# Kernel optimization log

Hardware: AMD Instinct MI355X
Metric: run time of the kernel (lower is better)

The kernel has to match this reference:

```python
import jax, jax.numpy as jnp
import numpy as np

B, C, HIMG, WIMG = 32, 3, 224, 224
P, D, L, F, H, NC = 16, 768, 12, 3072, 12, 1000
S = (HIMG // P) * (WIMG // P)  # 196 tokens
DH = D // H                    # 64 per head


def setup_inputs() -> dict:
    key = jax.random.key(0)
    ks = jax.random.split(key, 12)
    rn = lambda i, shape, sc: jax.random.normal(ks[i], shape, jnp.float32) * sc
    return dict(
        x=rn(0, (B, C, HIMG, WIMG), 1.0),
        conv_w=rn(1, (D, C, P, P), 0.02),
        conv_b=jnp.zeros((D,), jnp.float32),
        pos_embed=rn(2, (S, D), 0.02),
        ln1_s=jnp.ones((L, D), jnp.float32),
        ln1_b=jnp.zeros((L, D), jnp.float32),
        wq=rn(3, (L, D, D), 0.02),
        wk=rn(4, (L, D, D), 0.02),
        wv=rn(5, (L, D, D), 0.02),
        ln2_s=jnp.ones((L, D), jnp.float32),
        ln2_b=jnp.zeros((L, D), jnp.float32),
        w1=rn(6, (L, D, F), 0.02),
        b1=jnp.zeros((L, F), jnp.float32),
        w2=rn(7, (L, F, D), 0.02),
        b2=jnp.zeros((L, D), jnp.float32),
        fc_w=rn(8, (D, NC), 0.02),
        fc_b=jnp.zeros((NC,), jnp.float32),
    )


def _layernorm(x, scale, bias, eps=1e-5):
    m = x.mean(-1, keepdims=True)
    v = ((x - m) ** 2).mean(-1, keepdims=True)
    return (x - m) * jax.lax.rsqrt(v + eps) * scale + bias


def reference(x, conv_w, conv_b, pos_embed, ln1_s, ln1_b, wq, wk, wv,
              ln2_s, ln2_b, w1, b1, w2, b2, fc_w, fc_b):
    # patch embedding: stride-P conv, then b c h w -> b (h w) c, add pos embed
    h = jax.lax.conv_general_dilated(
        x, conv_w, (P, P), 'VALID',
        dimension_numbers=('NCHW', 'OIHW', 'NCHW'))
    h = h + conv_b[None, :, None, None]
    h = h.reshape(B, D, S).transpose(0, 2, 1) + pos_embed  # [B,S,D]

    # NOTE: original scales attention logits by 1/sqrt(seq_len), not 1/sqrt(d_head)
    scale = 1.0 / jnp.sqrt(jnp.float32(S))

    def layer(hx, p):
        l1s, l1b, Wq, Wk, Wv, l2s, l2b, W1, B1, W2, B2 = p
        xn = _layernorm(hx, l1s, l1b)
        q = (xn @ Wq).reshape(B, S, H, DH)
        k = (xn @ Wk).reshape(B, S, H, DH)
        v = (xn @ Wv).reshape(B, S, H, DH)
        att = jax.nn.softmax(jnp.einsum('bshd,bthd->bhst', q, k) * scale, axis=-1)
        o = jnp.einsum('bhst,bthd->bshd', att, v).reshape(B, S, D)
        hx = hx + o
        y = _layernorm(hx, l2s, l2b) @ W1 + B1
        y = jax.nn.gelu(y, approximate=False) @ W2 + B2
        return hx + y, None

    h, _ = jax.lax.scan(layer, h, (ln1_s, ln1_b, wq, wk, wv,
                                   ln2_s, ln2_b, w1, b1, w2, b2))
    return h.mean(axis=1) @ fc_w + fc_b  # [B, num_classes]
```

## Files before the change

kernel.cpp:

```cpp
#include <hip/hip_runtime.h>
#include <hip/hip_bf16.h>

typedef __attribute__((ext_vector_type(8))) short bf16x8;
typedef __attribute__((ext_vector_type(4))) short bf16x4;
typedef __attribute__((ext_vector_type(4))) float f32x4;

#define DEVI static __device__ __forceinline__

DEVI unsigned short f2bf(float f) {
  __hip_bfloat16 h = __float2bfloat16(f);
  return __builtin_bit_cast(unsigned short, h);
}

DEVI f32x4 mfma16(bf16x8 a, bf16x8 b, f32x4 c) {
  return __builtin_amdgcn_mfma_f32_16x16x32_bf16(a, b, c, 0, 0, 0);
}

DEVI void gload16(const unsigned short* g, unsigned short* l) {
  __builtin_amdgcn_global_load_lds(
      (const __attribute__((address_space(1))) void*)g,
      (__attribute__((address_space(3))) void*)l, 16, 0, 0);
}

__global__ __launch_bounds__(256) void k_im2col(const float* __restrict__ x,
                                                unsigned short* __restrict__ A) {
  int t = blockIdx.x * 256 + threadIdx.x;
  int m = t / 192;
  int qq = t - m * 192;
  int kk = qq * 4;
  int c = kk >> 8;
  int r = kk & 255;
  int i = r >> 4;
  int j = r & 15;
  int b = m / 196;
  int s = m - b * 196;
  int ph = s / 14;
  int pw = s - ph * 14;
  const float* src = x + ((size_t)((b * 3 + c) * 224 + ph * 16 + i)) * 224 + pw * 16 + j;
  f32x4 v = *reinterpret_cast<const f32x4*>(src);
  bf16x4 o;
  o[0] = (short)f2bf(v[0]); o[1] = (short)f2bf(v[1]);
  o[2] = (short)f2bf(v[2]); o[3] = (short)f2bf(v[3]);
  *reinterpret_cast<bf16x4*>(A + (size_t)m * 768 + kk) = o;
}

__global__ __launch_bounds__(256) void k_cvt(const float* __restrict__ in,
                                             unsigned short* __restrict__ out) {
  int t = blockIdx.x * 256 + threadIdx.x;
  f32x4 v = *reinterpret_cast<const f32x4*>(in + (size_t)t * 4);
  bf16x4 o;
  o[0] = (short)f2bf(v[0]); o[1] = (short)f2bf(v[1]);
  o[2] = (short)f2bf(v[2]); o[3] = (short)f2bf(v[3]);
  *reinterpret_cast<bf16x4*>(out + (size_t)t * 4) = o;
}

DEVI void transpose_tile(const float* __restrict__ in, unsigned short* __restrict__ out,
                         int K, int N, int kt, int nt, unsigned short (*tile)[68]) {
  int r = threadIdx.x >> 4;
  int c4 = (threadIdx.x & 15) * 4;
  int k0 = kt * 64, n0 = nt * 64;
#pragma unroll
  for (int rr0 = 0; rr0 < 4; rr0++) {
    int rr = r + rr0 * 16;
    f32x4 v = *reinterpret_cast<const f32x4*>(in + (size_t)(k0 + rr) * N + n0 + c4);
    bf16x4 o;
    o[0] = (short)f2bf(v[0]); o[1] = (short)f2bf(v[1]);
    o[2] = (short)f2bf(v[2]); o[3] = (short)f2bf(v[3]);
    *reinterpret_cast<bf16x4*>(&tile[rr][c4]) = o;
  }
  __syncthreads();
#pragma unroll
  for (int rr0 = 0; rr0 < 4; rr0++) {
    int rr = r + rr0 * 16;
    bf16x4 o;
    o[0] = (short)tile[c4 + 0][rr];
    o[1] = (short)tile[c4 + 1][rr];
    o[2] = (short)tile[c4 + 2][rr];
    o[3] = (short)tile[c4 + 3][rr];
    *reinterpret_cast<bf16x4*>(out + (size_t)(n0 + rr) * K + k0 + c4) = o;
  }
}

__global__ __launch_bounds__(256) void k_wconvert(
    const float* __restrict__ wq, const float* __restrict__ wk, const float* __restrict__ wv,
    const float* __restrict__ w1, const float* __restrict__ w2,
    unsigned short* __restrict__ wqkvT, unsigned short* __restrict__ w1T,
    unsigned short* __restrict__ w2T) {
  __shared__ unsigned short tile[64][68];
  int bid = blockIdx.x;
  if (bid < 432) {
    int mm = bid / 144, t2 = bid - mm * 144;
    const float* in = (mm == 0) ? wq : ((mm == 1) ? wk : wv);
    transpose_tile(in, wqkvT + (size_t)mm * 768 * 768, 768, 768, t2 / 12, t2 % 12, tile);
  } else if (bid < 1008) {
    int t2 = bid - 432;
    transpose_tile(w1, w1T, 768, 3072, t2 / 48, t2 % 48, tile);
  } else {
    int t2 = bid - 1008;
    transpose_tile(w2, w2T, 3072, 768, t2 / 12, t2 % 12, tile);
  }
}

__global__ __launch_bounds__(256) void k_ln(const float* __restrict__ h,
                                            const float* __restrict__ sc,
                                            const float* __restrict__ bi,
                                            unsigned short* __restrict__ xn) {
  int wave = threadIdx.x >> 6, lane = threadIdx.x & 63;
  int row = blockIdx.x * 4 + wave;
  const float* hr = h + (size_t)row * 768;
  f32x4 v[3];
  float sum = 0.f;
#pragma unroll
  for (int i = 0; i < 3; i++) {
    v[i] = *reinterpret_cast<const f32x4*>(hr + i * 256 + lane * 4);
    sum += v[i][0] + v[i][1] + v[i][2] + v[i][3];
  }
#pragma unroll
  for (int m = 1; m < 64; m <<= 1) sum += __shfl_xor(sum, m, 64);
  float mean = sum * (1.f / 768.f);
  float var = 0.f;
#pragma unroll
  for (int i = 0; i < 3; i++)
#pragma unroll
    for (int c = 0; c < 4; c++) { float d = v[i][c] - mean; var += d * d; }
#pragma unroll
  for (int m = 1; m < 64; m <<= 1) var += __shfl_xor(var, m, 64);
  float rs = rsqrtf(var * (1.f / 768.f) + 1e-5f);
#pragma unroll
  for (int i = 0; i < 3; i++) {
    int col = i * 256 + lane * 4;
    f32x4 s4 = *reinterpret_cast<const f32x4*>(sc + col);
    f32x4 b4 = *reinterpret_cast<const f32x4*>(bi + col);
    bf16x4 o;
#pragma unroll
    for (int c = 0; c < 4; c++) o[c] = (short)f2bf((v[i][c] - mean) * rs * s4[c] + b4[c]);
    *reinterpret_cast<bf16x4*>(xn + (size_t)row * 768 + col) = o;
  }
}

template <int EPI>
__global__ __launch_bounds__(256) void k_gemm(
    const unsigned short* __restrict__ A, const unsigned short* __restrict__ Bt, int K,
    const float* __restrict__ bias, const float* __restrict__ aux,
    float* __restrict__ outF, unsigned short* __restrict__ outB) {
  __shared__ __align__(16) unsigned short As[128 * 32];
  __shared__ __align__(16) unsigned short Bs[128 * 32];
  int m0 = blockIdx.y * 128, n0 = blockIdx.x * 128;
  int tid = threadIdx.x;
  int wave = tid >> 6, lane = tid & 63;
  int wm = (wave >> 1) * 64, wn = (wave & 1) * 64;
  int lr = lane & 15, lg = lane >> 4;

  f32x4 acc[4][4];
  const f32x4 fz = {0.f, 0.f, 0.f, 0.f};
#pragma unroll
  for (int i = 0; i < 4; i++)
#pragma unroll
    for (int j = 0; j < 4; j++) acc[i][j] = fz;

  int srow = wave * 16 + (lane >> 2);
  int scol = (lane & 3) * 8;
  const unsigned short* Ag = A + (size_t)(m0 + srow) * K + scol;
  const unsigned short* Bg = Bt + (size_t)(n0 + srow) * K + scol;
  unsigned short* Al = &As[wave * 16 * 32];
  unsigned short* Bl = &Bs[wave * 16 * 32];

  int nk = K >> 5;
  for (int kt = 0; kt < nk; kt++) {
    int k0 = kt << 5;
#pragma unroll
    for (int j = 0; j < 2; j++) {
      gload16(Ag + (size_t)j * 64 * K + k0, Al + j * 64 * 32);
      gload16(Bg + (size_t)j * 64 * K + k0, Bl + j * 64 * 32);
    }
    __syncthreads();
    bf16x8 a[4], b[4];
#pragma unroll
    for (int i = 0; i < 4; i++) {
      a[i] = *reinterpret_cast<const bf16x8*>(&As[(wm + i * 16 + lr) * 32 + lg * 8]);
      b[i] = *reinterpret_cast<const bf16x8*>(&Bs[(wn + i * 16 + lr) * 32 + lg * 8]);
    }
#pragma unroll
    for (int mi = 0; mi < 4; mi++)
#pragma unroll
      for (int ni = 0; ni < 4; ni++) acc[mi][ni] = mfma16(a[mi], b[ni], acc[mi][ni]);
    __syncthreads();
  }

#pragma unroll
  for (int mi = 0; mi < 4; mi++) {
#pragma unroll
    for (int ni = 0; ni < 4; ni++) {
#pragma unroll
      for (int r = 0; r < 4; r++) {
        int m = m0 + wm + mi * 16 + lg * 4 + r;
        int n = n0 + wn + ni * 16 + lr;
        float val = acc[mi][ni][r];
        if (EPI == 0) {
          int s = m % 196;
          outF[(size_t)m * 768 + n] = val + bias[n] + aux[(size_t)s * 768 + n];
        } else if (EPI == 1) {
          int bb = m / 196, s = m - bb * 196;
          int which = n / 768, n7 = n - which * 768;
          int hd = n7 >> 6, dh = n7 & 63;
          outB[(size_t)which * 4816896 + ((size_t)((bb * 12 + hd) * 196 + s) << 6) + dh] =
              f2bf(val);
        } else if (EPI == 2) {
          float tt = val + bias[n];
          float g = 0.5f * tt * (1.f + erff(tt * 0.70710678118654752f));
          outB[(size_t)m * 3072 + n] = f2bf(g);
        } else {
          outF[(size_t)m * 768 + n] += val + bias[n];
        }
      }
    }
  }
}

__global__ __launch_bounds__(256) void k_attn(const unsigned short* __restrict__ q,
                                              const unsigned short* __restrict__ k,
                                              const unsigned short* __restrict__ v,
                                              float* __restrict__ h) {
  __shared__ __align__(16) unsigned short Kl[208][72];
  __shared__ __align__(16) unsigned short Vt[64][248];
  __shared__ __align__(16) unsigned short Sc[4][16][232];
  int bh = blockIdx.x;
  int b = bh / 12, hh = bh - b * 12;
  size_t base = (size_t)bh * 196 * 64;
  int tid = threadIdx.x, wave = tid >> 6, lane = tid & 63;
  int lr = lane & 15, lg = lane >> 4;

  const bf16x8 bz = {0, 0, 0, 0, 0, 0, 0, 0};
  for (int u = tid; u < 208 * 8; u += 256) {
    int row = u >> 3, c8 = (u & 7) * 8;
    bf16x8 val = bz;
    if (row < 196) val = *reinterpret_cast<const bf16x8*>(k + base + row * 64 + c8);
    *reinterpret_cast<bf16x8*>(&Kl[row][c8]) = val;
  }
  for (int u = tid; u < 224 * 8; u += 256) {
    int t = u >> 3, d8 = (u & 7) * 8;
    bf16x8 val = bz;
    if (t < 196) val = *reinterpret_cast<const bf16x8*>(v + base + t * 64 + d8);
#pragma unroll
    for (int i = 0; i < 8; i++) Vt[d8 + i][t] = (unsigned short)val[i];
  }
  for (int i2 = lane; i2 < 256; i2 += 64) Sc[wave][i2 >> 4][208 + (i2 & 15)] = 0;
  __syncthreads();

  const float scale = 1.f / 14.f;
  for (int st = wave; st < 13; st += 4) {
    int qb = st * 16;
    int s = qb + lr;
    bf16x8 aq0 = bz, aq1 = bz;
    if (s < 196) {
      aq0 = *reinterpret_cast<const bf16x8*>(q + base + (size_t)s * 64 + lg * 8);
      aq1 = *reinterpret_cast<const bf16x8*>(q + base + (size_t)s * 64 + 32 + lg * 8);
    }
    f32x4 sc[13];
#pragma unroll
    for (int t = 0; t < 13; t++) {
      bf16x8 bk0 = *reinterpret_cast<const bf16x8*>(&Kl[t * 16 + lr][lg * 8]);
      bf16x8 bk1 = *reinterpret_cast<const bf16x8*>(&Kl[t * 16 + lr][32 + lg * 8]);
      f32x4 z = {0.f, 0.f, 0.f, 0.f};
      z = mfma16(aq0, bk0, z);
      z = mfma16(aq1, bk1, z);
      sc[t] = z;
    }
    float mx[4] = {-1e30f, -1e30f, -1e30f, -1e30f};
#pragma unroll
    for (int t = 0; t < 13; t++) {
      int tc = t * 16 + lr;
#pragma unroll
      for (int r = 0; r < 4; r++) {
        float xv = (tc < 196) ? sc[t][r] * scale : -1e30f;
        sc[t][r] = xv;
        mx[r] = fmaxf(mx[r], xv);
      }
    }
#pragma unroll
    for (int r = 0; r < 4; r++)
#pragma unroll
      for (int mm = 1; mm < 16; mm <<= 1) mx[r] = fmaxf(mx[r], __shfl_xor(mx[r], mm, 64));
    float sm[4] = {0.f, 0.f, 0.f, 0.f};
#pragma unroll
    for (int t = 0; t < 13; t++)
#pragma unroll
      for (int r = 0; r < 4; r++) {
        float e = __expf(sc[t][r] - mx[r]);
        sc[t][r] = e;
        sm[r] += e;
      }
#pragma unroll
    for (int r = 0; r < 4; r++)
#pragma unroll
      for (int mm = 1; mm < 16; mm <<= 1) sm[r] += __shfl_xor(sm[r], mm, 64);
    float inv[4];
#pragma unroll
    for (int r = 0; r < 4; r++) inv[r] = 1.f / sm[r];
#pragma unroll
    for (int t = 0; t < 13; t++)
#pragma unroll
      for (int r = 0; r < 4; r++)
        Sc[wave][lg * 4 + r][t * 16 + lr] = f2bf(sc[t][r] * inv[r]);
    asm volatile("s_waitcnt lgkmcnt(0)" ::: "memory");
    bf16x8 ap[7];
#pragma unroll
    for (int ks = 0; ks < 7; ks++)
      ap[ks] = *reinterpret_cast<const bf16x8*>(&Sc[wave][lr][ks * 32 + lg * 8]);
#pragma unroll
    for (int nt = 0; nt < 4; nt++) {
      f32x4 o = {0.f, 0.f, 0.f, 0.f};
#pragma unroll
      for (int ks = 0; ks < 7; ks++) {
        bf16x8 bv = *reinterpret_cast<const bf16x8*>(&Vt[nt * 16 + lr][ks * 32 + lg * 8]);
        o = mfma16(ap[ks], bv, o);
      }
#pragma unroll
      for (int r = 0; r < 4; r++) {
        int s2 = qb + lg * 4 + r;
        if (s2 < 196) h[(size_t)(b * 196 + s2) * 768 + hh * 64 + nt * 16 + lr] += o[r];
      }
    }
  }
}

__global__ __launch_bounds__(256) void k_mean(const float* __restrict__ h,
                                              float* __restrict__ hm) {
  int b = blockIdx.x, d = blockIdx.y * 256 + threadIdx.x;
  float acc = 0.f;
  for (int s = 0; s < 196; s++) acc += h[(size_t)(b * 196 + s) * 768 + d];
  hm[b * 768 + d] = acc * (1.f / 196.f);
}

__global__ __launch_bounds__(256) void k_fc(const float* __restrict__ hm,
                                            const float* __restrict__ w,
                                            const float* __restrict__ bias,
                                            float* __restrict__ out) {
  int b = blockIdx.x, n = blockIdx.y * 256 + threadIdx.x;
  if (n >= 1000) return;
  float acc = bias[n];
  for (int d = 0; d < 768; d++) acc += hm[b * 768 + d] * w[d * 1000 + n];
  out[b * 1000 + n] = acc;
}

extern "C" void kernel_launch(void* const* d_in, const int* in_sizes, int n_in,
                              void* d_out, int out_size, void* d_ws, size_t ws_size,
                              hipStream_t stream) {
  const float* x      = (const float*)d_in[0];
  const float* conv_w = (const float*)d_in[1];
  const float* conv_b = (const float*)d_in[2];
  const float* pos    = (const float*)d_in[3];
  const float* ln1_s  = (const float*)d_in[4];
  const float* ln1_b  = (const float*)d_in[5];
  const float* wq     = (const float*)d_in[6];
  const float* wk     = (const float*)d_in[7];
  const float* wv     = (const float*)d_in[8];
  const float* ln2_s  = (const float*)d_in[9];
  const float* ln2_b  = (const float*)d_in[10];
  const float* w1     = (const float*)d_in[11];
  const float* b1     = (const float*)d_in[12];
  const float* w2     = (const float*)d_in[13];
  const float* b2     = (const float*)d_in[14];
  const float* fc_w   = (const float*)d_in[15];
  const float* fc_b   = (const float*)d_in[16];
  float* out = (float*)d_out;

  char* p = (char*)d_ws;
  auto alloc = [&](size_t bytes) {
    char* r = p;
    p += (bytes + 255) & ~(size_t)255;
    return r;
  };
  const size_t M = 6272, QSZ = 4816896;
  float* h              = (float*)alloc(M * 768 * 4);
  unsigned short* xn    = (unsigned short*)alloc(M * 768 * 2);
  unsigned short* qkv   = (unsigned short*)alloc(3 * QSZ * 2);
  unsigned short* y1    = (unsigned short*)alloc(M * 3072 * 2);
  unsigned short* wqkvT = (unsigned short*)alloc((size_t)2304 * 768 * 2);
  unsigned short* w1T   = (unsigned short*)alloc((size_t)3072 * 768 * 2);
  unsigned short* w2T   = (unsigned short*)alloc((size_t)3072 * 768 * 2);
  unsigned short* cwB   = (unsigned short*)alloc((size_t)768 * 768 * 2);
  float* hm             = (float*)alloc(32 * 768 * 4);

  k_cvt<<<576, 256, 0, stream>>>(conv_w, cwB);
  k_im2col<<<4704, 256, 0, stream>>>(x, xn);
  k_gemm<0><<<dim3(6, 49), 256, 0, stream>>>(xn, cwB, 768, conv_b, pos, h, nullptr);

  for (int l = 0; l < 12; l++) {
    k_wconvert<<<1584, 256, 0, stream>>>(
        wq + (size_t)l * 589824, wk + (size_t)l * 589824, wv + (size_t)l * 589824,
        w1 + (size_t)l * 2359296, w2 + (size_t)l * 2359296, wqkvT, w1T, w2T);
    k_ln<<<1568, 256, 0, stream>>>(h, ln1_s + l * 768, ln1_b + l * 768, xn);
    k_gemm<1><<<dim3(18, 49), 256, 0, stream>>>(xn, wqkvT, 768, nullptr, nullptr, nullptr, qkv);
    k_attn<<<384, 256, 0, stream>>>(qkv, qkv + QSZ, qkv + 2 * QSZ, h);
    k_ln<<<1568, 256, 0, stream>>>(h, ln2_s + l * 768, ln2_b + l * 768, xn);
    k_gemm<2><<<dim3(24, 49), 256, 0, stream>>>(xn, w1T, 768, b1 + (size_t)l * 3072, nullptr,
                                                nullptr, y1);
    k_gemm<3><<<dim3(6, 49), 256, 0, stream>>>(y1, w2T, 3072, b2 + (size_t)l * 768, nullptr, h,
                                               nullptr);
  }
  k_mean<<<dim3(32, 3), 256, 0, stream>>>(h, hm);
  k_fc<<<dim3(32, 4), 256, 0, stream>>>(hm, fc_w, fc_b, out);
}
```

Baseline: 3.339 ms.

## Double-buffer GEMM LDS tiles, remap blocks for XCD locality, cheaper epilogue

Moves the GEMM main loop to two LDS buffers so the next K-tile's global-to-LDS load is issued before the MFMAs on the current tile, with one barrier per step instead of two. Remaps block indices so consecutive tiles land on the same XCD and are grouped along M for better L2 reuse. The epilogue computes div/mod by 196 once per row group instead of per element, and the exact erff in GELU is replaced by an Abramowitz-Stegun polynomial approximation. The erf approximation has about 1e-7 absolute error, which could slightly change numerics, and doubling LDS may reduce occupancy.

```diff
diff --git a/kernel.cpp b/kernel.cpp
--- a/kernel.cpp
+++ b/kernel.cpp
@@ -20,6 +20,16 @@
   __builtin_amdgcn_global_load_lds(
       (const __attribute__((address_space(1))) void*)g,
       (__attribute__((address_space(3))) void*)l, 16, 0, 0);
+}
+
+DEVI float erf_fast(float x) {
+  float ax = fabsf(x);
+  float t = 1.f / (1.f + 0.3275911f * ax);
+  float poly = ((((1.061405429f * t - 1.453152027f) * t + 1.421413741f) * t -
+                 0.284496736f) * t + 0.254829592f) * t;
+  float e = __expf(-x * x);
+  float er = 1.f - poly * e;
+  return copysignf(er, x);
 }
 
 __global__ __launch_bounds__(256) void k_im2col(const float* __restrict__ x,
@@ -143,9 +153,25 @@
     const unsigned short* __restrict__ A, const unsigned short* __restrict__ Bt, int K,
     const float* __restrict__ bias, const float* __restrict__ aux,
     float* __restrict__ outF, unsigned short* __restrict__ outB) {
-  __shared__ __align__(16) unsigned short As[128 * 32];
-  __shared__ __align__(16) unsigned short Bs[128 * 32];
-  int m0 = blockIdx.y * 128, n0 = blockIdx.x * 128;
+  __shared__ __align__(16) unsigned short As[2][128 * 32];
+  __shared__ __align__(16) unsigned short Bs[2][128 * 32];
+
+  int GX = gridDim.x, GY = gridDim.y;
+  int nb = GX * GY;
+  int lin = blockIdx.y * GX + blockIdx.x;
+  int q = nb >> 3, r8 = nb & 7;
+  int xcd = lin & 7, off = lin >> 3;
+  int wid = (xcd < r8 ? xcd * (q + 1) : r8 * (q + 1) + (xcd - r8) * q) + off;
+  const int GM = 8;
+  int per = GM * GX;
+  int g = wid / per;
+  int first_m = g * GM;
+  int gm = min(GM, GY - first_m);
+  int rem = wid - g * per;
+  int mt = first_m + rem % gm;
+  int nt = rem / gm;
+  int m0 = mt * 128, n0 = nt * 128;
+
   int tid = threadIdx.x;
   int wave = tid >> 6, lane = tid & 63;
   int wm = (wave >> 1) * 64, wn = (wave & 1) * 64;
@@ -162,23 +188,29 @@
   int scol = (lane & 3) * 8;
   const unsigned short* Ag = A + (size_t)(m0 + srow) * K + scol;
   const unsigned short* Bg = Bt + (size_t)(n0 + srow) * K + scol;
-  unsigned short* Al = &As[wave * 16 * 32];
-  unsigned short* Bl = &Bs[wave * 16 * 32];
+  int lofs = wave * 16 * 32;
 
   int nk = K >> 5;
-  for (int kt = 0; kt < nk; kt++) {
-    int k0 = kt << 5;
+#pragma unroll
+  for (int j = 0; j < 2; j++) {
+    gload16(Ag + (size_t)j * 64 * K, &As[0][lofs + j * 64 * 32]);
+    gload16(Bg + (size_t)j * 64 * K, &Bs[0][lofs + j * 64 * 32]);
+  }
+  __syncthreads();
+
+  for (int kt = 0; kt < nk - 1; kt++) {
+    int cur = kt & 1;
+    int k0 = (kt + 1) << 5;
 #pragma unroll
     for (int j = 0; j < 2; j++) {
-      gload16(Ag + (size_t)j * 64 * K + k0, Al + j * 64 * 32);
-      gload16(Bg + (size_t)j * 64 * K + k0, Bl + j * 64 * 32);
-    }
-    __syncthreads();
+      gload16(Ag + (size_t)j * 64 * K + k0, &As[cur ^ 1][lofs + j * 64 * 32]);
+      gload16(Bg + (size_t)j * 64 * K + k0, &Bs[cur ^ 1][lofs + j * 64 * 32]);
+    }
     bf16x8 a[4], b[4];
 #pragma unroll
     for (int i = 0; i < 4; i++) {
-      a[i] = *reinterpret_cast<const bf16x8*>(&As[(wm + i * 16 + lr) * 32 + lg * 8]);
-      b[i] = *reinterpret_cast<const bf16x8*>(&Bs[(wn + i * 16 + lr) * 32 + lg * 8]);
+      a[i] = *reinterpret_cast<const bf16x8*>(&As[cur][(wm + i * 16 + lr) * 32 + lg * 8]);
+      b[i] = *reinterpret_cast<const bf16x8*>(&Bs[cur][(wn + i * 16 + lr) * 32 + lg * 8]);
     }
 #pragma unroll
     for (int mi = 0; mi < 4; mi++)
@@ -186,31 +218,66 @@
       for (int ni = 0; ni < 4; ni++) acc[mi][ni] = mfma16(a[mi], b[ni], acc[mi][ni]);
     __syncthreads();
   }
-
-#pragma unroll
-  for (int mi = 0; mi < 4; mi++) {
+  {
+    int cur = (nk - 1) & 1;
+    bf16x8 a[4], b[4];
+#pragma unroll
+    for (int i = 0; i < 4; i++) {
+      a[i] = *reinterpret_cast<const bf16x8*>(&As[cur][(wm + i * 16 + lr) * 32 + lg * 8]);
+      b[i] = *reinterpret_cast<const bf16x8*>(&Bs[cur][(wn + i * 16 + lr) * 32 + lg * 8]);
+    }
+#pragma unroll
+    for (int mi = 0; mi < 4; mi++)
+#pragma unroll
+      for (int ni = 0; ni < 4; ni++) acc[mi][ni] = mfma16(a[mi], b[ni], acc[mi][ni]);
+  }
+
+  if (EPI == 1) {
 #pragma unroll
     for (int ni = 0; ni < 4; ni++) {
-#pragma unroll
-      for (int r = 0; r < 4; r++) {
-        int m = m0 + wm + mi * 16 + lg * 4 + r;
+      int n = n0 + wn + ni * 16 + lr;
+      int which = (n >= 1536) ? 2 : ((n >= 768) ? 1 : 0);
+      int n7 = n - which * 768;
+      int hd = n7 >> 6, dh = n7 & 63;
+      unsigned short* ob = outB + (size_t)which * 4816896 + dh;
+#pragma unroll
+      for (int mi = 0; mi < 4; mi++) {
+        int mb = m0 + wm + mi * 16 + lg * 4;
+        int bb = mb / 196;
+        int s = mb - bb * 196;
+#pragma unroll
+        for (int r = 0; r < 4; r++) {
+          ob[((size_t)((bb * 12 + hd) * 196 + s) << 6)] = f2bf(acc[mi][ni][r]);
+          s++;
+          if (s == 196) { s = 0; bb++; }
+        }
+      }
+    }
+  } else {
+#pragma unroll
+    for (int mi = 0; mi < 4; mi++) {
+      int mb = m0 + wm + mi * 16 + lg * 4;
+      int bb = mb / 196;
+      int s0 = mb - bb * 196;
+#pragma unroll
+      for (int ni = 0; ni < 4; ni++) {
         int n = n0 + wn + ni * 16 + lr;
-        float val = acc[mi][ni][r];
-        if (EPI == 0) {
-          int s = m % 196;
-          outF[(size_t)m * 768 + n] = val + bias[n] + aux[(size_t)s * 768 + n];
-        } else if (EPI == 1) {
-          int bb = m / 196, s = m - bb * 196;
-          int which = n / 768, n7 = n - which * 768;
-          int hd = n7 >> 6, dh = n7 & 63;
-          outB[(size_t)which * 4816896 + ((size_t)((bb * 12 + hd) * 196 + s) << 6) + dh] =
-              f2bf(val);
-        } else if (EPI == 2) {
-          float tt = val + bias[n];
-          float g = 0.5f * tt * (1.f + erff(tt * 0.70710678118654752f));
-          outB[(size_t)m * 3072 + n] = f2bf(g);
-        } else {
-          outF[(size_t)m * 768 + n] += val + bias[n];
+        int s = s0;
+#pragma unroll
+        for (int r = 0; r < 4; r++) {
+          int m = mb + r;
+          float val = acc[mi][ni][r];
+          if (EPI == 0) {
+            outF[(size_t)m * 768 + n] = val + bias[n] + aux[(size_t)s * 768 + n];
+            s++;
+            if (s == 196) s = 0;
+          } else if (EPI == 2) {
+            float u = val + bias[n];
+            float gg = 0.5f * u * (1.f + erf_fast(u * 0.70710678118654752f));
+            outB[(size_t)m * 3072 + n] = f2bf(gg);
+          } else {
+            outF[(size_t)m * 768 + n] += val + bias[n];
+          }
         }
       }
     }
```

New measurement: 3.274 ms. No clear change (-2.0%).
